# Optimization experiments

Hardware: AMD Instinct MI355X
Metric: run time of the kernel (lower is better)

Reference implementation:

```python
import jax, jax.numpy as jnp
import numpy as np

KNN = 10       # knn_size
TOPK = 4       # top_k_select
H = 4          # num_heads
HID = 64       # edge-MLP hidden dim


def setup_inputs() -> dict:
    key = jax.random.key(0)
    ks = jax.random.split(key, 12)
    B, V, D = 4, 4096, 256
    s = 0.02
    return {
        "voxel_tokens": jax.random.normal(ks[0], (B, V, D), jnp.float32),
        "voxel_coords": jax.random.uniform(ks[1], (B, V, 3), jnp.float32) * 10.0,
        "mask": jnp.ones((B, V), dtype=bool),
        # EdgeScoringMLP: Linear(2D+3 -> 64), Linear(64 -> 1)
        "W1": jax.random.normal(ks[2], (2 * D + 3, HID), jnp.float32) * s,
        "b1": jnp.zeros((HID,), jnp.float32),
        "W2": jax.random.normal(ks[3], (HID, 1), jnp.float32) * s,
        "b2": jnp.zeros((1,), jnp.float32),
        # CrossAttention projections (D -> D)
        "Wq": jax.random.normal(ks[4], (D, D), jnp.float32) * s,
        "bq": jnp.zeros((D,), jnp.float32),
        "Wk": jax.random.normal(ks[5], (D, D), jnp.float32) * s,
        "bk": jnp.zeros((D,), jnp.float32),
        "Wv": jax.random.normal(ks[6], (D, D), jnp.float32) * s,
        "bv": jnp.zeros((D,), jnp.float32),
        "Wo": jax.random.normal(ks[7], (D, D), jnp.float32) * s,
        "bo": jnp.zeros((D,), jnp.float32),
    }


def reference(voxel_tokens, voxel_coords, mask,
              W1, b1, W2, b2, Wq, bq, Wk, bk, Wv, bv, Wo, bo):
    # mask is all-True (Vp == V per batch element), so the original per-batch
    # loop over dynamic voxel counts is an exact vmap over B. Dropouts are in
    # eval mode (identity).
    D = voxel_tokens.shape[-1]
    Dh = D // H

    def single(tok, coo):  # tok: (V, D), coo: (V, 3)
        # --- KNN graph build (squared euclidean; monotonic in true cdist) ---
        sq = jnp.sum(coo * coo, axis=-1)                        # (V,)
        d2 = sq[:, None] + sq[None, :] - 2.0 * (coo @ coo.T)    # (V, V)
        _, knn = jax.lax.top_k(-d2, KNN + 1)                    # smallest dists
        knn = knn[:, 1:]                                        # drop self, (V, KNN)

        # --- edge features: [anchor_tok, neighbor_tok, rel_pos] ---
        nb_tok = tok[knn]                                       # (V, KNN, D)
        rel = coo[knn] - coo[:, None, :]                        # (V, KNN, 3)
        anchor = jnp.broadcast_to(tok[:, None, :], nb_tok.shape)
        ef = jnp.concatenate([anchor, nb_tok, rel], axis=-1)    # (V, KNN, 2D+3)

        # --- edge-MLP scoring + softmax + top-k edge select ---
        sc = (jax.nn.relu(ef @ W1 + b1) @ W2 + b2)[..., 0]      # (V, KNN)
        aw = jax.nn.softmax(sc, axis=-1)
        _, loc = jax.lax.top_k(aw, TOPK)                        # (V, TOPK)
        sel = jnp.take_along_axis(knn, loc, axis=-1)            # (V, TOPK)
        nbr = tok[sel]                                          # (V, TOPK, D)

        # --- cross attention over selected neighbors ---
        Q = (tok @ Wq + bq).reshape(-1, H, Dh)                  # (V, H, Dh)
        K = (nbr @ Wk + bk).reshape(-1, TOPK, H, Dh)            # (V, TOPK, H, Dh)
        Vv = (nbr @ Wv + bv).reshape(-1, TOPK, H, Dh)
        att = jnp.einsum('vhd,vshd->vhs', Q, K) / jnp.sqrt(jnp.float32(Dh))
        w = jax.nn.softmax(att, axis=-1)                        # (V, H, TOPK)
        out = jnp.einsum('vhs,vshd->vhd', w, Vv).reshape(-1, D)
        return out @ Wo + bo                                    # (V, D)

    return jax.vmap(single)(voxel_tokens, voxel_coords)        # (B, V, D)
```

## Files before the change

kernel.cpp:

```cpp
#include <hip/hip_runtime.h>
#include <hip/hip_bf16.h>

#define VV 4096
#define DDIM 256
#define KNN_K 10
#define TK 4

__device__ __forceinline__ float f_sq3(float x, float y, float z) {
    return __fadd_rn(__fadd_rn(__fmul_rn(x, x), __fmul_rn(y, y)), __fmul_rn(z, z));
}
__device__ __forceinline__ float f_dot3(float ax, float ay, float az,
                                        float bx, float by, float bz) {
    float d = __fmul_rn(ax, bx);
    d = __fmaf_rn(ay, by, d);
    d = __fmaf_rn(az, bz, d);
    return d;
}

__device__ __forceinline__ float f_d2(const float* __restrict__ cb, int j, float sqj,
                                      float qx, float qy, float qz, float sqq) {
    float xj = cb[j * 3 + 0], yj = cb[j * 3 + 1], zj = cb[j * 3 + 2];
    float dt = f_dot3(qx, qy, qz, xj, yj, zj);
    return __fsub_rn(__fadd_rn(sqq, sqj), __fmul_rn(2.0f, dt));
}

__device__ __forceinline__ unsigned long long mkkey(float d2, int j) {
    unsigned u = __float_as_uint(d2);
    u ^= (unsigned)((int)u >> 31) | 0x80000000u;
    return ((unsigned long long)u << 32) | (unsigned)j;
}

__global__ void __launch_bounds__(256) an_gemm_kernel(
    const float* __restrict__ tok,
    const float* __restrict__ W1,
    const float* __restrict__ coords,
    float* __restrict__ AN,
    float* __restrict__ sq)
{
    __shared__ float As[16][68];
    __shared__ float Bs[16][68];

    const int mBlock = blockIdx.x * 64;
    const int grp    = blockIdx.y;
    const float* W   = W1 + (size_t)grp * 256 * 64;

    const int tid = threadIdx.x;

    if (grp == 0 && tid < 64) {
        int m = mBlock + tid;
        sq[m] = f_sq3(coords[m * 3 + 0], coords[m * 3 + 1], coords[m * 3 + 2]);
    }

    const int tx = tid & 15;
    const int ty = tid >> 4;

    const int ar  = tid >> 2;
    const int ac4 = tid & 3;
    const int br  = tid >> 4;
    const int bc4 = tid & 15;

    float acc[4][4] = {};

    for (int k0 = 0; k0 < 256; k0 += 16) {
        float4 a4 = *(const float4*)&tok[(size_t)(mBlock + ar) * 256 + k0 + ac4 * 4];
        As[ac4 * 4 + 0][ar] = a4.x;
        As[ac4 * 4 + 1][ar] = a4.y;
        As[ac4 * 4 + 2][ar] = a4.z;
        As[ac4 * 4 + 3][ar] = a4.w;
        float4 b4 = *(const float4*)&W[(size_t)(k0 + br) * 64 + bc4 * 4];
        *(float4*)&Bs[br][bc4 * 4] = b4;
        __syncthreads();
        #pragma unroll
        for (int kk = 0; kk < 16; kk++) {
            float4 av = *(const float4*)&As[kk][ty * 4];
            float4 bv4 = *(const float4*)&Bs[kk][tx * 4];
            acc[0][0] = fmaf(av.x, bv4.x, acc[0][0]); acc[0][1] = fmaf(av.x, bv4.y, acc[0][1]);
            acc[0][2] = fmaf(av.x, bv4.z, acc[0][2]); acc[0][3] = fmaf(av.x, bv4.w, acc[0][3]);
            acc[1][0] = fmaf(av.y, bv4.x, acc[1][0]); acc[1][1] = fmaf(av.y, bv4.y, acc[1][1]);
            acc[1][2] = fmaf(av.y, bv4.z, acc[1][2]); acc[1][3] = fmaf(av.y, bv4.w, acc[1][3]);
            acc[2][0] = fmaf(av.z, bv4.x, acc[2][0]); acc[2][1] = fmaf(av.z, bv4.y, acc[2][1]);
            acc[2][2] = fmaf(av.z, bv4.z, acc[2][2]); acc[2][3] = fmaf(av.z, bv4.w, acc[2][3]);
            acc[3][0] = fmaf(av.w, bv4.x, acc[3][0]); acc[3][1] = fmaf(av.w, bv4.y, acc[3][1]);
            acc[3][2] = fmaf(av.w, bv4.z, acc[3][2]); acc[3][3] = fmaf(av.w, bv4.w, acc[3][3]);
        }
        __syncthreads();
    }

    #pragma unroll
    for (int i = 0; i < 4; i++) {
        int m = mBlock + ty * 4 + i;
        float4 o;
        o.x = acc[i][0]; o.y = acc[i][1]; o.z = acc[i][2]; o.w = acc[i][3];
        *(float4*)&AN[(size_t)m * 128 + grp * 64 + tx * 4] = o;
    }
}

__global__ void __launch_bounds__(256) knn_score_kernel(
    const float* __restrict__ AN,
    const float* __restrict__ coords,
    const float* __restrict__ sq,
    const float* __restrict__ W1,
    const float* __restrict__ b1,
    const float* __restrict__ W2,
    int* __restrict__ sel)
{
    const int tid  = threadIdx.x;
    const int lane = tid & 63;
    const int wave = tid >> 6;
    const int q    = blockIdx.x * 4 + wave;
    const int b    = q >> 12;
    const int v    = q & 4095;
    const int base = q & ~4095;
    const float* cb  = coords + (size_t)b * VV * 3;
    const float* sqb = sq + base;

    __shared__ int   sKnn[4][KNN_K];
    __shared__ float sHid[4][KNN_K][65];
    __shared__ float sSc[4][KNN_K];

    const float qx = cb[v * 3 + 0];
    const float qy = cb[v * 3 + 1];
    const float qz = cb[v * 3 + 2];
    const float sqq = f_sq3(qx, qy, qz);

    unsigned long long best   = ~0ull;
    unsigned long long second = ~0ull;
    unsigned long long used   = 0ull;

    #pragma unroll 4
    for (int i = 0; i < 64; i++) {
        int j = i * 64 + lane;
        unsigned long long k = mkkey(f_d2(cb, j, sqb[j], qx, qy, qz, sqq), j);
        if (k < best) { second = best; best = k; }
        else if (k < second) { second = k; }
    }

    #pragma unroll 1
    for (int it = 0; it < 11; it++) {
        unsigned long long rb = best;
        #pragma unroll
        for (int off = 1; off < 64; off <<= 1) {
            unsigned olo = __shfl_xor((unsigned)rb, off);
            unsigned ohi = __shfl_xor((unsigned)(rb >> 32), off);
            unsigned long long o = ((unsigned long long)ohi << 32) | olo;
            if (o < rb) rb = o;
        }
        int wj = (int)((unsigned)rb & 4095u);
        if (it >= 1 && lane == 0) sKnn[wave][it - 1] = wj;

        if ((unsigned)best == (unsigned)rb) {
            used |= 1ull << (wj >> 6);
            best = second;
            second = ~0ull;
            if (best == ~0ull) {
                #pragma unroll 1
                for (int i = 0; i < 64; i++) {
                    if ((used >> i) & 1ull) continue;
                    int j = i * 64 + lane;
                    unsigned long long k = mkkey(f_d2(cb, j, sqb[j], qx, qy, qz, sqq), j);
                    if (k < best) { second = best; best = k; }
                    else if (k < second) { second = k; }
                }
            }
        }
    }

    const float sAl = AN[(size_t)q * 128 + lane];
    const float b1l = b1[lane];
    const float wr0 = W1[(512 + 0) * 64 + lane];
    const float wr1 = W1[(512 + 1) * 64 + lane];
    const float wr2 = W1[(512 + 2) * 64 + lane];

    #pragma unroll 1
    for (int nb = 0; nb < KNN_K; nb++) {
        int kn = sKnn[wave][nb];
        float acc = __fadd_rn(sAl, AN[(size_t)(base + kn) * 128 + 64 + lane]);
        float rel0 = __fsub_rn(cb[kn * 3 + 0], qx);
        acc = __fmaf_rn(rel0, wr0, acc);
        float rel1 = __fsub_rn(cb[kn * 3 + 1], qy);
        acc = __fmaf_rn(rel1, wr1, acc);
        float rel2 = __fsub_rn(cb[kn * 3 + 2], qz);
        acc = __fmaf_rn(rel2, wr2, acc);
        float hid = __fadd_rn(acc, b1l);
        sHid[wave][nb][lane] = hid > 0.0f ? hid : 0.0f;
    }

    if (lane < KNN_K) {
        float s = 0.0f;
        #pragma unroll 8
        for (int h = 0; h < 64; h++)
            s = __fmaf_rn(sHid[wave][lane][h], W2[h], s);
        sSc[wave][lane] = s;
    }

    if (lane == 0) {
        unsigned um = 0;
        #pragma unroll
        for (int s = 0; s < TK; s++) {
            float bests = -3.4e38f; int bj = 0;
            for (int jj = 0; jj < KNN_K; jj++) {
                if (um & (1u << jj)) continue;
                if (sSc[wave][jj] > bests) { bests = sSc[wave][jj]; bj = jj; }
            }
            um |= 1u << bj;
            sel[(size_t)q * TK + s] = base + sKnn[wave][bj];
        }
    }
}

__global__ void __launch_bounds__(256) qkv_gemm_kernel(
    const float* __restrict__ tok,
    const float* __restrict__ Wq, const float* __restrict__ bq,
    const float* __restrict__ Wk, const float* __restrict__ bk,
    const float* __restrict__ Wv, const float* __restrict__ bv,
    float* __restrict__ qkv)
{
    __shared__ float As[16][68];
    __shared__ float Bs[16][68];

    const int mBlock = blockIdx.x * 64;
    const int nBlock = blockIdx.y * 64;
    const int grp = nBlock >> 8;
    const int nIn = nBlock & 255;
    const float* W    = (grp == 0) ? Wq : (grp == 1) ? Wk : Wv;
    const float* bias = (grp == 0) ? bq : (grp == 1) ? bk : bv;

    const int tid = threadIdx.x;
    const int tx = tid & 15;
    const int ty = tid >> 4;

    const int ar  = tid >> 2;
    const int ac4 = tid & 3;
    const int br  = tid >> 4;
    const int bc4 = tid & 15;

    float acc[4][4] = {};

    for (int k0 = 0; k0 < 256; k0 += 16) {
        float4 a4 = *(const float4*)&tok[(size_t)(mBlock + ar) * 256 + k0 + ac4 * 4];
        As[ac4 * 4 + 0][ar] = a4.x;
        As[ac4 * 4 + 1][ar] = a4.y;
        As[ac4 * 4 + 2][ar] = a4.z;
        As[ac4 * 4 + 3][ar] = a4.w;
        float4 b4 = *(const float4*)&W[(size_t)(k0 + br) * 256 + nIn + bc4 * 4];
        *(float4*)&Bs[br][bc4 * 4] = b4;
        __syncthreads();
        #pragma unroll
        for (int kk = 0; kk < 16; kk++) {
            float4 av = *(const float4*)&As[kk][ty * 4];
            float4 bv4 = *(const float4*)&Bs[kk][tx * 4];
            acc[0][0] = fmaf(av.x, bv4.x, acc[0][0]); acc[0][1] = fmaf(av.x, bv4.y, acc[0][1]);
            acc[0][2] = fmaf(av.x, bv4.z, acc[0][2]); acc[0][3] = fmaf(av.x, bv4.w, acc[0][3]);
            acc[1][0] = fmaf(av.y, bv4.x, acc[1][0]); acc[1][1] = fmaf(av.y, bv4.y, acc[1][1]);
            acc[1][2] = fmaf(av.y, bv4.z, acc[1][2]); acc[1][3] = fmaf(av.y, bv4.w, acc[1][3]);
            acc[2][0] = fmaf(av.z, bv4.x, acc[2][0]); acc[2][1] = fmaf(av.z, bv4.y, acc[2][1]);
            acc[2][2] = fmaf(av.z, bv4.z, acc[2][2]); acc[2][3] = fmaf(av.z, bv4.w, acc[2][3]);
            acc[3][0] = fmaf(av.w, bv4.x, acc[3][0]); acc[3][1] = fmaf(av.w, bv4.y, acc[3][1]);
            acc[3][2] = fmaf(av.w, bv4.z, acc[3][2]); acc[3][3] = fmaf(av.w, bv4.w, acc[3][3]);
        }
        __syncthreads();
    }

    #pragma unroll
    for (int i = 0; i < 4; i++) {
        int m = mBlock + ty * 4 + i;
        float4 o;
        o.x = acc[i][0] + bias[nIn + tx * 4 + 0];
        o.y = acc[i][1] + bias[nIn + tx * 4 + 1];
        o.z = acc[i][2] + bias[nIn + tx * 4 + 2];
        o.w = acc[i][3] + bias[nIn + tx * 4 + 3];
        *(float4*)&qkv[(size_t)m * 768 + nBlock + tx * 4] = o;
    }
}

__global__ void __launch_bounds__(256) attn_gather_kernel(
    const float* __restrict__ qkv, const int* __restrict__ sel,
    float* __restrict__ attnout)
{
    const int q = blockIdx.x;
    const int tid = threadIdx.x;

    const float qv = qkv[(size_t)q * 768 + tid];

    int rows[TK];
    #pragma unroll
    for (int s = 0; s < TK; s++) rows[s] = sel[(size_t)q * TK + s];

    float att[TK];
    #pragma unroll
    for (int s = 0; s < TK; s++) {
        float p = qv * qkv[(size_t)rows[s] * 768 + 256 + tid];
        #pragma unroll
        for (int m = 1; m < 64; m <<= 1) p += __shfl_xor(p, m);
        att[s] = p * 0.125f;
    }

    float mx  = fmaxf(fmaxf(att[0], att[1]), fmaxf(att[2], att[3]));
    float e0 = expf(att[0] - mx), e1 = expf(att[1] - mx),
          e2 = expf(att[2] - mx), e3 = expf(att[3] - mx);
    float inv = 1.0f / (e0 + e1 + e2 + e3);

    float o = (e0 * qkv[(size_t)rows[0] * 768 + 512 + tid] +
               e1 * qkv[(size_t)rows[1] * 768 + 512 + tid] +
               e2 * qkv[(size_t)rows[2] * 768 + 512 + tid] +
               e3 * qkv[(size_t)rows[3] * 768 + 512 + tid]) * inv;

    attnout[(size_t)q * 256 + tid] = o;
}

__global__ void __launch_bounds__(256) wo_gemm_kernel(
    const float* __restrict__ A,
    const float* __restrict__ Wo, const float* __restrict__ bo,
    float* __restrict__ out)
{
    __shared__ float As[16][68];
    __shared__ float Bs[16][68];

    const int mBlock = blockIdx.x * 64;
    const int nBlock = blockIdx.y * 64;

    const int tid = threadIdx.x;
    const int tx = tid & 15;
    const int ty = tid >> 4;

    const int ar  = tid >> 2;
    const int ac4 = tid & 3;
    const int br  = tid >> 4;
    const int bc4 = tid & 15;

    float acc[4][4] = {};

    for (int k0 = 0; k0 < 256; k0 += 16) {
        float4 a4 = *(const float4*)&A[(size_t)(mBlock + ar) * 256 + k0 + ac4 * 4];
        As[ac4 * 4 + 0][ar] = a4.x;
        As[ac4 * 4 + 1][ar] = a4.y;
        As[ac4 * 4 + 2][ar] = a4.z;
        As[ac4 * 4 + 3][ar] = a4.w;
        float4 b4 = *(const float4*)&Wo[(size_t)(k0 + br) * 256 + nBlock + bc4 * 4];
        *(float4*)&Bs[br][bc4 * 4] = b4;
        __syncthreads();
        #pragma unroll
        for (int kk = 0; kk < 16; kk++) {
            float4 av = *(const float4*)&As[kk][ty * 4];
            float4 bv4 = *(const float4*)&Bs[kk][tx * 4];
            acc[0][0] = fmaf(av.x, bv4.x, acc[0][0]); acc[0][1] = fmaf(av.x, bv4.y, acc[0][1]);
            acc[0][2] = fmaf(av.x, bv4.z, acc[0][2]); acc[0][3] = fmaf(av.x, bv4.w, acc[0][3]);
            acc[1][0] = fmaf(av.y, bv4.x, acc[1][0]); acc[1][1] = fmaf(av.y, bv4.y, acc[1][1]);
            acc[1][2] = fmaf(av.y, bv4.z, acc[1][2]); acc[1][3] = fmaf(av.y, bv4.w, acc[1][3]);
            acc[2][0] = fmaf(av.z, bv4.x, acc[2][0]); acc[2][1] = fmaf(av.z, bv4.y, acc[2][1]);
            acc[2][2] = fmaf(av.z, bv4.z, acc[2][2]); acc[2][3] = fmaf(av.z, bv4.w, acc[2][3]);
            acc[3][0] = fmaf(av.w, bv4.x, acc[3][0]); acc[3][1] = fmaf(av.w, bv4.y, acc[3][1]);
            acc[3][2] = fmaf(av.w, bv4.z, acc[3][2]); acc[3][3] = fmaf(av.w, bv4.w, acc[3][3]);
        }
        __syncthreads();
    }

    #pragma unroll
    for (int i = 0; i < 4; i++) {
        int m = mBlock + ty * 4 + i;
        float4 o;
        o.x = acc[i][0] + bo[nBlock + tx * 4 + 0];
        o.y = acc[i][1] + bo[nBlock + tx * 4 + 1];
        o.z = acc[i][2] + bo[nBlock + tx * 4 + 2];
        o.w = acc[i][3] + bo[nBlock + tx * 4 + 3];
        *(float4*)&out[(size_t)m * 256 + nBlock + tx * 4] = o;
    }
}

__global__ void __launch_bounds__(256) fused_voxel_attn(
    const float* __restrict__ tok,
    const float* __restrict__ coords,
    const float* __restrict__ W1,
    const float* __restrict__ b1,
    const float* __restrict__ W2,
    const float* __restrict__ Wq, const float* __restrict__ bq,
    const float* __restrict__ Wk, const float* __restrict__ bk,
    const float* __restrict__ Wv, const float* __restrict__ bv,
    const float* __restrict__ Wo, const float* __restrict__ bo,
    float* __restrict__ out, int out_size)
{
    const int q    = blockIdx.x;
    const int b    = q >> 12;
    const int v    = q & 4095;
    const int base = q & ~4095;
    const int tid  = threadIdx.x;
    const float* cb = coords + (size_t)b * VV * 3;

    __shared__ float  sval[256];
    __shared__ int    sidx[256];
    __shared__ int    sKnn[KNN_K];
    __shared__ int    sSel[TK];
    __shared__ float  sTokA[DDIM];
    __shared__ float  sTokN[KNN_K][DDIM];
    __shared__ float  sAH[64];
    __shared__ float  sHid[KNN_K][64];
    __shared__ float  sSc[KNN_K];
    __shared__ float  sP[TK][256];
    __shared__ float  sAtt[4][TK];
    __shared__ float  sO[DDIM];

    const float qx = cb[v * 3 + 0];
    const float qy = cb[v * 3 + 1];
    const float qz = cb[v * 3 + 2];
    const float sqq = f_sq3(qx, qy, qz);

    float d2[16];
    #pragma unroll
    for (int i = 0; i < 16; i++) {
        int j = tid + i * 256;
        float xj = cb[j * 3 + 0], yj = cb[j * 3 + 1], zj = cb[j * 3 + 2];
        float sqj = f_sq3(xj, yj, zj);
        float dt  = f_dot3(qx, qy, qz, xj, yj, zj);
        d2[i] = __fsub_rn(__fadd_rn(sqq, sqj), __fmul_rn(2.0f, dt));
    }

    unsigned used = 0;
    for (int it = 0; it < 11; it++) {
        float best = 3.4e38f;
// ... 136 lines not shown
                                65536LL, 256LL, 65536LL, 256LL,
                                65536LL, 256LL, 65536LL, 256LL};
    int idx[13];
    const int n = n_in;

    const long long* s64 = (const long long*)(const void*)in_sizes;
    const int*       s32 = in_sizes;

    bool ok = false;

    if (n >= 13 && s64[0] == want[0]) {
        ok = true;
        int walk = 0;
        for (int t = 0; t < 13; t++) {
            int f = -1;
            for (int i = walk; i < n; i++) {
                if (s64[i] == want[t]) { f = i; break; }
            }
            if (f < 0) { ok = false; break; }
            idx[t] = f; walk = f + 1;
        }
    }

    if (!ok) {
        ok = true;
        int walk = 0;
        for (int t = 0; t < 13; t++) {
            int f = -1;
            for (int i = walk; i < n; i++) {
                if ((long long)s32[i] == want[t]) { f = i; break; }
            }
            if (f < 0) { ok = false; break; }
            idx[t] = f; walk = f + 1;
        }
    }

    if (!ok) return;

    const float* tok    = (const float*)d_in[idx[0]];
    const float* coords = (const float*)d_in[idx[1]];
    const float* W1     = (const float*)d_in[idx[2]];
    const float* b1     = (const float*)d_in[idx[3]];
    const float* W2     = (const float*)d_in[idx[4]];
    const float* Wq     = (const float*)d_in[idx[5]];
    const float* bq     = (const float*)d_in[idx[6]];
    const float* Wk     = (const float*)d_in[idx[7]];
    const float* bk     = (const float*)d_in[idx[8]];
    const float* Wv     = (const float*)d_in[idx[9]];
    const float* bv     = (const float*)d_in[idx[10]];
    const float* Wo     = (const float*)d_in[idx[11]];
    const float* bo     = (const float*)d_in[idx[12]];
    float* out = (float*)d_out;

    const size_t NEED = 67436544;
    if (ws_size >= NEED) {
        char* ws = (char*)d_ws;
        int*   sel     = (int*)  (ws + 0);
        float* AN      = (float*)(ws + 262144);
        float* attnout = (float*)(ws + 262144);
        float* qkv     = (float*)(ws + 17039360);
        float* sq      = (float*)(ws + 67371008);

        an_gemm_kernel<<<dim3(256, 2), dim3(256), 0, stream>>>(tok, W1, coords, AN, sq);
        knn_score_kernel<<<dim3(4096), dim3(256), 0, stream>>>(AN, coords, sq, W1, b1, W2, sel);
        qkv_gemm_kernel<<<dim3(256, 12), dim3(256), 0, stream>>>(tok, Wq, bq, Wk, bk, Wv, bv, qkv);
        attn_gather_kernel<<<dim3(16384), dim3(256), 0, stream>>>(qkv, sel, attnout);
        wo_gemm_kernel<<<dim3(256, 4), dim3(256), 0, stream>>>(attnout, Wo, bo, out);
    } else {
        fused_voxel_attn<<<dim3(16384), dim3(256), 0, stream>>>(
            tok, coords, W1, b1, W2, Wq, bq, Wk, bk, Wv, bv, Wo, bo, out, out_size);
    }
}
```

Before: 373.0 us.

## Merge KNN scoring and QKV GEMM into one launch, pack coords as float4

Packs each voxel's coordinates and squared norm into a single float4 so the brute-force KNN scan does one vector load per candidate instead of four scalar loads. The KNN/scoring blocks and the QKV projection GEMM become one heterogeneous kernel, interleaving 16 KNN blocks with 3 GEMM blocks per group so the compute-heavy GEMM can overlap the latency-bound KNN scan. The QKV and Wo GEMMs switch from 64x64 to 128x128 tiles with 2x2 register sub-tiles for more reuse per shared-memory load. The cost is higher register pressure in the merged kernel, which may lower occupancy for the KNN path, and fewer blocks for the Wo GEMM.

```diff
diff --git a/kernel.cpp b/kernel.cpp
--- a/kernel.cpp
+++ b/kernel.cpp
@@ -17,13 +17,6 @@
     return d;
 }
 
-__device__ __forceinline__ float f_d2(const float* __restrict__ cb, int j, float sqj,
-                                      float qx, float qy, float qz, float sqq) {
-    float xj = cb[j * 3 + 0], yj = cb[j * 3 + 1], zj = cb[j * 3 + 2];
-    float dt = f_dot3(qx, qy, qz, xj, yj, zj);
-    return __fsub_rn(__fadd_rn(sqq, sqj), __fmul_rn(2.0f, dt));
-}
-
 __device__ __forceinline__ unsigned long long mkkey(float d2, int j) {
     unsigned u = __float_as_uint(d2);
     u ^= (unsigned)((int)u >> 31) | 0x80000000u;
@@ -35,7 +28,7 @@
     const float* __restrict__ W1,
     const float* __restrict__ coords,
     float* __restrict__ AN,
-    float* __restrict__ sq)
+    float4* __restrict__ cxyzs)
 {
     __shared__ float As[16][68];
     __shared__ float Bs[16][68];
@@ -48,7 +41,8 @@
 
     if (grp == 0 && tid < 64) {
         int m = mBlock + tid;
-        sq[m] = f_sq3(coords[m * 3 + 0], coords[m * 3 + 1], coords[m * 3 + 2]);
+        float x = coords[m * 3 + 0], y = coords[m * 3 + 1], z = coords[m * 3 + 2];
+        cxyzs[m] = make_float4(x, y, z, f_sq3(x, y, z));
     }
 
     const int tx = tid & 15;
@@ -95,181 +89,204 @@
     }
 }
 
-__global__ void __launch_bounds__(256) knn_score_kernel(
+__global__ void __launch_bounds__(256) knn_qkv_kernel(
     const float* __restrict__ AN,
-    const float* __restrict__ coords,
-    const float* __restrict__ sq,
+    const float4* __restrict__ cxyzs,
     const float* __restrict__ W1,
     const float* __restrict__ b1,
     const float* __restrict__ W2,
-    int* __restrict__ sel)
-{
-    const int tid  = threadIdx.x;
-    const int lane = tid & 63;
-    const int wave = tid >> 6;
-    const int q    = blockIdx.x * 4 + wave;
-    const int b    = q >> 12;
-    const int v    = q & 4095;
-    const int base = q & ~4095;
-    const float* cb  = coords + (size_t)b * VV * 3;
-    const float* sqb = sq + base;
-
-    __shared__ int   sKnn[4][KNN_K];
-    __shared__ float sHid[4][KNN_K][65];
-    __shared__ float sSc[4][KNN_K];
-
-    const float qx = cb[v * 3 + 0];
-    const float qy = cb[v * 3 + 1];
-    const float qz = cb[v * 3 + 2];
-    const float sqq = f_sq3(qx, qy, qz);
-
-    unsigned long long best   = ~0ull;
-    unsigned long long second = ~0ull;
-    unsigned long long used   = 0ull;
-
-    #pragma unroll 4
-    for (int i = 0; i < 64; i++) {
-        int j = i * 64 + lane;
-        unsigned long long k = mkkey(f_d2(cb, j, sqb[j], qx, qy, qz, sqq), j);
-        if (k < best) { second = best; best = k; }
-        else if (k < second) { second = k; }
-    }
-
-    #pragma unroll 1
-    for (int it = 0; it < 11; it++) {
-        unsigned long long rb = best;
-        #pragma unroll
-        for (int off = 1; off < 64; off <<= 1) {
-            unsigned olo = __shfl_xor((unsigned)rb, off);
-            unsigned ohi = __shfl_xor((unsigned)(rb >> 32), off);
-            unsigned long long o = ((unsigned long long)ohi << 32) | olo;
-            if (o < rb) rb = o;
-        }
-        int wj = (int)((unsigned)rb & 4095u);
-        if (it >= 1 && lane == 0) sKnn[wave][it - 1] = wj;
-
-        if ((unsigned)best == (unsigned)rb) {
-            used |= 1ull << (wj >> 6);
-            best = second;
-            second = ~0ull;
-            if (best == ~0ull) {
-                #pragma unroll 1
-                for (int i = 0; i < 64; i++) {
-                    if ((used >> i) & 1ull) continue;
-                    int j = i * 64 + lane;
-                    unsigned long long k = mkkey(f_d2(cb, j, sqb[j], qx, qy, qz, sqq), j);
-                    if (k < best) { second = best; best = k; }
-                    else if (k < second) { second = k; }
-                }
-            }
-        }
-    }
-
-    const float sAl = AN[(size_t)q * 128 + lane];
-    const float b1l = b1[lane];
-    const float wr0 = W1[(512 + 0) * 64 + lane];
-    const float wr1 = W1[(512 + 1) * 64 + lane];
-    const float wr2 = W1[(512 + 2) * 64 + lane];
-
-    #pragma unroll 1
-    for (int nb = 0; nb < KNN_K; nb++) {
-        int kn = sKnn[wave][nb];
-        float acc = __fadd_rn(sAl, AN[(size_t)(base + kn) * 128 + 64 + lane]);
-        float rel0 = __fsub_rn(cb[kn * 3 + 0], qx);
-        acc = __fmaf_rn(rel0, wr0, acc);
-        float rel1 = __fsub_rn(cb[kn * 3 + 1], qy);
-        acc = __fmaf_rn(rel1, wr1, acc);
-        float rel2 = __fsub_rn(cb[kn * 3 + 2], qz);
-        acc = __fmaf_rn(rel2, wr2, acc);
-        float hid = __fadd_rn(acc, b1l);
-        sHid[wave][nb][lane] = hid > 0.0f ? hid : 0.0f;
-    }
-
-    if (lane < KNN_K) {
-        float s = 0.0f;
-        #pragma unroll 8
-        for (int h = 0; h < 64; h++)
-            s = __fmaf_rn(sHid[wave][lane][h], W2[h], s);
-        sSc[wave][lane] = s;
-    }
-
-    if (lane == 0) {
-        unsigned um = 0;
-        #pragma unroll
-        for (int s = 0; s < TK; s++) {
-            float bests = -3.4e38f; int bj = 0;
-            for (int jj = 0; jj < KNN_K; jj++) {
-                if (um & (1u << jj)) continue;
-                if (sSc[wave][jj] > bests) { bests = sSc[wave][jj]; bj = jj; }
-            }
-            um |= 1u << bj;
-            sel[(size_t)q * TK + s] = base + sKnn[wave][bj];
-        }
-    }
-}
-
-__global__ void __launch_bounds__(256) qkv_gemm_kernel(
+    int* __restrict__ sel,
     const float* __restrict__ tok,
     const float* __restrict__ Wq, const float* __restrict__ bq,
     const float* __restrict__ Wk, const float* __restrict__ bk,
     const float* __restrict__ Wv, const float* __restrict__ bv,
     float* __restrict__ qkv)
 {
-    __shared__ float As[16][68];
-    __shared__ float Bs[16][68];
-
-    const int mBlock = blockIdx.x * 64;
-    const int nBlock = blockIdx.y * 64;
-    const int grp = nBlock >> 8;
-    const int nIn = nBlock & 255;
-    const float* W    = (grp == 0) ? Wq : (grp == 1) ? Wk : Wv;
-    const float* bias = (grp == 0) ? bq : (grp == 1) ? bk : bv;
-
-    const int tid = threadIdx.x;
-    const int tx = tid & 15;
-    const int ty = tid >> 4;
-
-    const int ar  = tid >> 2;
-    const int ac4 = tid & 3;
-    const int br  = tid >> 4;
-    const int bc4 = tid & 15;
-
-    float acc[4][4] = {};
-
-    for (int k0 = 0; k0 < 256; k0 += 16) {
-        float4 a4 = *(const float4*)&tok[(size_t)(mBlock + ar) * 256 + k0 + ac4 * 4];
-        As[ac4 * 4 + 0][ar] = a4.x;
-        As[ac4 * 4 + 1][ar] = a4.y;
-        As[ac4 * 4 + 2][ar] = a4.z;
-        As[ac4 * 4 + 3][ar] = a4.w;
-        float4 b4 = *(const float4*)&W[(size_t)(k0 + br) * 256 + nIn + bc4 * 4];
-        *(float4*)&Bs[br][bc4 * 4] = b4;
-        __syncthreads();
-        #pragma unroll
-        for (int kk = 0; kk < 16; kk++) {
-            float4 av = *(const float4*)&As[kk][ty * 4];
-            float4 bv4 = *(const float4*)&Bs[kk][tx * 4];
-            acc[0][0] = fmaf(av.x, bv4.x, acc[0][0]); acc[0][1] = fmaf(av.x, bv4.y, acc[0][1]);
-            acc[0][2] = fmaf(av.x, bv4.z, acc[0][2]); acc[0][3] = fmaf(av.x, bv4.w, acc[0][3]);
-            acc[1][0] = fmaf(av.y, bv4.x, acc[1][0]); acc[1][1] = fmaf(av.y, bv4.y, acc[1][1]);
-            acc[1][2] = fmaf(av.y, bv4.z, acc[1][2]); acc[1][3] = fmaf(av.y, bv4.w, acc[1][3]);
-            acc[2][0] = fmaf(av.z, bv4.x, acc[2][0]); acc[2][1] = fmaf(av.z, bv4.y, acc[2][1]);
-            acc[2][2] = fmaf(av.z, bv4.z, acc[2][2]); acc[2][3] = fmaf(av.z, bv4.w, acc[2][3]);
-            acc[3][0] = fmaf(av.w, bv4.x, acc[3][0]); acc[3][1] = fmaf(av.w, bv4.y, acc[3][1]);
-            acc[3][2] = fmaf(av.w, bv4.z, acc[3][2]); acc[3][3] = fmaf(av.w, bv4.w, acc[3][3]);
-        }
-        __syncthreads();
-    }
-
-    #pragma unroll
-    for (int i = 0; i < 4; i++) {
-        int m = mBlock + ty * 4 + i;
-        float4 o;
-        o.x = acc[i][0] + bias[nIn + tx * 4 + 0];
-        o.y = acc[i][1] + bias[nIn + tx * 4 + 1];
-        o.z = acc[i][2] + bias[nIn + tx * 4 + 2];
-        o.w = acc[i][3] + bias[nIn + tx * 4 + 3];
-        *(float4*)&qkv[(size_t)m * 768 + nBlock + tx * 4] = o;
+    __shared__ __align__(16) char smem[16896];
+    const int tid   = threadIdx.x;
+    const int g     = blockIdx.x;
+    const int group = g / 19;
+    const int rem   = g - group * 19;
+
+    if (rem < 16) {
+        const int kb   = group * 16 + rem;
+        const int lane = tid & 63;
+        const int wave = tid >> 6;
+        const int q    = kb * 4 + wave;
+        const int base = q & ~4095;
+        const int v    = q & 4095;
+        const float4* cx = cxyzs + base;
+
+        int*   sKnn = (int*)smem;
+        float* sSc  = (float*)(smem + 160);
+        float* sHid = (float*)(smem + 320);
+
+        float4 cq = cx[v];
+        const float qx = cq.x, qy = cq.y, qz = cq.z, sqq = cq.w;
+
+        unsigned long long best   = ~0ull;
+        unsigned long long second = ~0ull;
+        unsigned long long used   = 0ull;
+
+        #pragma unroll 4
+        for (int i = 0; i < 64; i++) {
+            int j = i * 64 + lane;
+            float4 c = cx[j];
+            float dt  = f_dot3(qx, qy, qz, c.x, c.y, c.z);
+            float d2v = __fsub_rn(__fadd_rn(sqq, c.w), __fmul_rn(2.0f, dt));
+            unsigned long long k = mkkey(d2v, j);
+            if (k < best) { second = best; best = k; }
+            else if (k < second) { second = k; }
+        }
+
+        #pragma unroll 1
+        for (int it = 0; it < 11; it++) {
+            unsigned long long rb = best;
+            #pragma unroll
+            for (int off = 1; off < 64; off <<= 1) {
+                unsigned olo = __shfl_xor((unsigned)rb, off);
+                unsigned ohi = __shfl_xor((unsigned)(rb >> 32), off);
+                unsigned long long o = ((unsigned long long)ohi << 32) | olo;
+                if (o < rb) rb = o;
+            }
+            int wj = (int)((unsigned)rb & 4095u);
+            if (it >= 1 && lane == 0) sKnn[wave * KNN_K + it - 1] = wj;
+
+            if ((unsigned)best == (unsigned)rb) {
+                used |= 1ull << (wj >> 6);
+                best = second;
+                second = ~0ull;
+                if (best == ~0ull) {
+                    #pragma unroll 1
+                    for (int i = 0; i < 64; i++) {
+                        if ((used >> i) & 1ull) continue;
+                        int j = i * 64 + lane;
+                        float4 c = cx[j];
+                        float dt  = f_dot3(qx, qy, qz, c.x, c.y, c.z);
+                        float d2v = __fsub_rn(__fadd_rn(sqq, c.w), __fmul_rn(2.0f, dt));
+                        unsigned long long k = mkkey(d2v, j);
+                        if (k < best) { second = best; best = k; }
+                        else if (k < second) { second = k; }
+                    }
+                }
+            }
+        }
+
+        const float sAl = AN[(size_t)q * 128 + lane];
+        const float b1l = b1[lane];
+        const float wr0 = W1[(512 + 0) * 64 + lane];
+        const float wr1 = W1[(512 + 1) * 64 + lane];
+        const float wr2 = W1[(512 + 2) * 64 + lane];
+
+        #pragma unroll 1
+        for (int nb = 0; nb < KNN_K; nb++) {
+            int kn = sKnn[wave * KNN_K + nb];
+            float4 cn = cx[kn];
+            float acc = __fadd_rn(sAl, AN[(size_t)(base + kn) * 128 + 64 + lane]);
+            float rel0 = __fsub_rn(cn.x, qx);
+            acc = __fmaf_rn(rel0, wr0, acc);
+            float rel1 = __fsub_rn(cn.y, qy);
+            acc = __fmaf_rn(rel1, wr1, acc);
+            float rel2 = __fsub_rn(cn.z, qz);
+            acc = __fmaf_rn(rel2, wr2, acc);
+            float hid = __fadd_rn(acc, b1l);
+            sHid[(wave * KNN_K + nb) * 65 + lane] = hid > 0.0f ? hid : 0.0f;
+        }
+
+        if (lane < KNN_K) {
+            float s = 0.0f;
+            #pragma unroll 8
+            for (int h = 0; h < 64; h++)
+                s = __fmaf_rn(sHid[(wave * KNN_K + lane) * 65 + h], W2[h], s);
+            sSc[wave * KNN_K + lane] = s;
+        }
+
+        if (lane == 0) {
+            unsigned um = 0;
+            #pragma unroll
+            for (int s = 0; s < TK; s++) {
+                float bests = -3.4e38f; int bj = 0;
+                for (int jj = 0; jj < KNN_K; jj++) {
+                    if (um & (1u << jj)) continue;
+                    float sc = sSc[wave * KNN_K + jj];
+                    if (sc > bests) { bests = sc; bj = jj; }
+                }
+                um |= 1u << bj;
+                sel[(size_t)q * TK + s] = base + sKnn[wave * KNN_K + bj];
+            }
+        }
+    } else {
+        float* As = (float*)smem;
+        float* Bs = (float*)smem + 16 * 132;
+
+        const int id     = group * 3 + (rem - 16);
+        const int mBlock = (id & 127) * 128;
+        const int nb     = id >> 7;
+        const int grp    = nb >> 1;
+        const int nIn    = (nb & 1) * 128;
+        const float* W    = (grp == 0) ? Wq : (grp == 1) ? Wk : Wv;
+        const float* bias = (grp == 0) ? bq : (grp == 1) ? bk : bv;
+
+        const int tx = tid & 15;
+        const int ty = tid >> 4;
+        const int ar  = tid >> 2;
+        const int ac4 = tid & 3;
+        const int br  = tid >> 4;
+        const int bc4 = tid & 15;
+
+        float acc[2][2][4][4] = {};
+
+        for (int k0 = 0; k0 < 256; k0 += 16) {
+            float4 a0 = *(const float4*)&tok[(size_t)(mBlock + ar) * 256 + k0 + ac4 * 4];
+            float4 a1 = *(const float4*)&tok[(size_t)(mBlock + 64 + ar) * 256 + k0 + ac4 * 4];
+            As[(ac4 * 4 + 0) * 132 + ar] = a0.x;      As[(ac4 * 4 + 0) * 132 + 64 + ar] = a1.x;
+            As[(ac4 * 4 + 1) * 132 + ar] = a0.y;      As[(ac4 * 4 + 1) * 132 + 64 + ar] = a1.y;
+            As[(ac4 * 4 + 2) * 132 + ar] = a0.z;      As[(ac4 * 4 + 2) * 132 + 64 + ar] = a1.z;
+            As[(ac4 * 4 + 3) * 132 + ar] = a0.w;      As[(ac4 * 4 + 3) * 132 + 64 + ar] = a1.w;
+            float4 b0 = *(const float4*)&W[(size_t)(k0 + br) * 256 + nIn + bc4 * 4];
+            float4 b1v = *(const float4*)&W[(size_t)(k0 + br) * 256 + nIn + 64 + bc4 * 4];
+            *(float4*)&Bs[br * 132 + bc4 * 4] = b0;
+            *(float4*)&Bs[br * 132 + 64 + bc4 * 4] = b1v;
+            __syncthreads();
+            #pragma unroll
+            for (int kk = 0; kk < 16; kk++) {
+                float4 av0 = *(const float4*)&As[kk * 132 + ty * 4];
+                float4 av1 = *(const float4*)&As[kk * 132 + 64 + ty * 4];
+                float4 bv0 = *(const float4*)&Bs[kk * 132 + tx * 4];
+                float4 bv1 = *(const float4*)&Bs[kk * 132 + 64 + tx * 4];
+                const float am[2][4] = {{av0.x, av0.y, av0.z, av0.w},
+                                        {av1.x, av1.y, av1.z, av1.w}};
+                const float bn[2][4] = {{bv0.x, bv0.y, bv0.z, bv0.w},
+                                        {bv1.x, bv1.y, bv1.z, bv1.w}};
+                #pragma unroll
+                for (int mi = 0; mi < 2; mi++)
+                #pragma unroll
+                for (int i = 0; i < 4; i++)
+                #pragma unroll
+                for (int ni = 0; ni < 2; ni++)
+                #pragma unroll
+                for (int j = 0; j < 4; j++)
+                    acc[mi][ni][i][j] = fmaf(am[mi][i], bn[ni][j], acc[mi][ni][i][j]);
+            }
+            __syncthreads();
+        }
+
+        #pragma unroll
+        for (int mi = 0; mi < 2; mi++)
+        #pragma unroll
+        for (int i = 0; i < 4; i++) {
+            int m = mBlock + mi * 64 + ty * 4 + i;
+            #pragma unroll
+            for (int ni = 0; ni < 2; ni++) {
+                int col = nIn + ni * 64 + tx * 4;
+                float4 o;
+                o.x = acc[mi][ni][i][0] + bias[col + 0];
+                o.y = acc[mi][ni][i][1] + bias[col + 1];
+                o.z = acc[mi][ni][i][2] + bias[col + 2];
+                o.w = acc[mi][ni][i][3] + bias[col + 3];
+                *(float4*)&qkv[(size_t)m * 768 + grp * 256 + col] = o;
+            }
+        }
     }
 }
 
@@ -313,57 +330,72 @@
     const float* __restrict__ Wo, const float* __restrict__ bo,
     float* __restrict__ out)
 {
-    __shared__ float As[16][68];
-    __shared__ float Bs[16][68];
-
-    const int mBlock = blockIdx.x * 64;
-    const int nBlock = blockIdx.y * 64;
+    __shared__ float As[16][132];
+    __shared__ float Bs[16][132];
+
+    const int mBlock = blockIdx.x * 128;
+    const int nBlock = blockIdx.y * 128;
 
     const int tid = threadIdx.x;
     const int tx = tid & 15;
     const int ty = tid >> 4;
-
     const int ar  = tid >> 2;
     const int ac4 = tid & 3;
     const int br  = tid >> 4;
     const int bc4 = tid & 15;
 
-    float acc[4][4] = {};
+    float acc[2][2][4][4] = {};
 
     for (int k0 = 0; k0 < 256; k0 += 16) {
-        float4 a4 = *(const float4*)&A[(size_t)(mBlock + ar) * 256 + k0 + ac4 * 4];
-        As[ac4 * 4 + 0][ar] = a4.x;
-        As[ac4 * 4 + 1][ar] = a4.y;
-        As[ac4 * 4 + 2][ar] = a4.z;
-        As[ac4 * 4 + 3][ar] = a4.w;
-        float4 b4 = *(const float4*)&Wo[(size_t)(k0 + br) * 256 + nBlock + bc4 * 4];
-        *(float4*)&Bs[br][bc4 * 4] = b4;
+        float4 a0 = *(const float4*)&A[(size_t)(mBlock + ar) * 256 + k0 + ac4 * 4];
+        float4 a1 = *(const float4*)&A[(size_t)(mBlock + 64 + ar) * 256 + k0 + ac4 * 4];
+        As[ac4 * 4 + 0][ar] = a0.x;      As[ac4 * 4 + 0][64 + ar] = a1.x;
+        As[ac4 * 4 + 1][ar] = a0.y;      As[ac4 * 4 + 1][64 + ar] = a1.y;
+        As[ac4 * 4 + 2][ar] = a0.z;      As[ac4 * 4 + 2][64 + ar] = a1.z;
+        As[ac4 * 4 + 3][ar] = a0.w;      As[ac4 * 4 + 3][64 + ar] = a1.w;
+        float4 b0 = *(const float4*)&Wo[(size_t)(k0 + br) * 256 + nBlock + bc4 * 4];
+        float4 b1v = *(const float4*)&Wo[(size_t)(k0 + br) * 256 + nBlock + 64 + bc4 * 4];
+        *(float4*)&Bs[br][bc4 * 4] = b0;
+        *(float4*)&Bs[br][64 + bc4 * 4] = b1v;
         __syncthreads();
         #pragma unroll
         for (int kk = 0; kk < 16; kk++) {
-            float4 av = *(const float4*)&As[kk][ty * 4];
-            float4 bv4 = *(const float4*)&Bs[kk][tx * 4];
-            acc[0][0] = fmaf(av.x, bv4.x, acc[0][0]); acc[0][1] = fmaf(av.x, bv4.y, acc[0][1]);
-            acc[0][2] = fmaf(av.x, bv4.z, acc[0][2]); acc[0][3] = fmaf(av.x, bv4.w, acc[0][3]);
-            acc[1][0] = fmaf(av.y, bv4.x, acc[1][0]); acc[1][1] = fmaf(av.y, bv4.y, acc[1][1]);
-            acc[1][2] = fmaf(av.y, bv4.z, acc[1][2]); acc[1][3] = fmaf(av.y, bv4.w, acc[1][3]);
-            acc[2][0] = fmaf(av.z, bv4.x, acc[2][0]); acc[2][1] = fmaf(av.z, bv4.y, acc[2][1]);
-            acc[2][2] = fmaf(av.z, bv4.z, acc[2][2]); acc[2][3] = fmaf(av.z, bv4.w, acc[2][3]);
-            acc[3][0] = fmaf(av.w, bv4.x, acc[3][0]); acc[3][1] = fmaf(av.w, bv4.y, acc[3][1]);
-            acc[3][2] = fmaf(av.w, bv4.z, acc[3][2]); acc[3][3] = fmaf(av.w, bv4.w, acc[3][3]);
+            float4 av0 = *(const float4*)&As[kk][ty * 4];
+            float4 av1 = *(const float4*)&As[kk][64 + ty * 4];
+            float4 bv0 = *(const float4*)&Bs[kk][tx * 4];
+            float4 bv1 = *(const float4*)&Bs[kk][64 + tx * 4];
+            const float am[2][4] = {{av0.x, av0.y, av0.z, av0.w},
+                                    {av1.x, av1.y, av1.z, av1.w}};
+            const float bn[2][4] = {{bv0.x, bv0.y, bv0.z, bv0.w},
+                                    {bv1.x, bv1.y, bv1.z, bv1.w}};
+            #pragma unroll
+            for (int mi = 0; mi < 2; mi++)
+            #pragma unroll
+            for (int i = 0; i < 4; i++)
+            #pragma unroll
+            for (int ni = 0; ni < 2; ni++)
+            #pragma unroll
+            for (int j = 0; j < 4; j++)
+                acc[mi][ni][i][j] = fmaf(am[mi][i], bn[ni][j], acc[mi][ni][i][j]);
         }
         __syncthreads();
     }
 
     #pragma unroll
+    for (int mi = 0; mi < 2; mi++)
+    #pragma unroll
     for (int i = 0; i < 4; i++) {
-        int m = mBlock + ty * 4 + i;
-        float4 o;
-        o.x = acc[i][0] + bo[nBlock + tx * 4 + 0];
-        o.y = acc[i][1] + bo[nBlock + tx * 4 + 1];
-        o.z = acc[i][2] + bo[nBlock + tx * 4 + 2];
-        o.w = acc[i][3] + bo[nBlock + tx * 4 + 3];
-        *(float4*)&out[(size_t)m * 256 + nBlock + tx * 4] = o;
+        int m = mBlock + mi * 64 + ty * 4 + i;
+        #pragma unroll
+        for (int ni = 0; ni < 2; ni++) {
+            int col = nBlock + ni * 64 + tx * 4;
+            float4 o;
+            o.x = acc[mi][ni][i][0] + bo[col + 0];
+            o.y = acc[mi][ni][i][1] + bo[col + 1];
+            o.z = acc[mi][ni][i][2] + bo[col + 2];
+            o.w = acc[mi][ni][i][3] + bo[col + 3];
+            *(float4*)&out[(size_t)m * 256 + col] = o;
+        }
     }
 }
 
@@ -606,20 +638,20 @@
     const float* bo     = (const float*)d_in[idx[12]];
     float* out = (float*)d_out;
 
-    const size_t NEED = 67436544;
+    const size_t NEED = 67633152;
     if (ws_size >= NEED) {
         char* ws = (char*)d_ws;
-        int*   sel     = (int*)  (ws + 0);
-        float* AN      = (float*)(ws + 262144);
-        float* attnout = (float*)(ws + 262144);
-        float* qkv     = (float*)(ws + 17039360);
-        float* sq      = (float*)(ws + 67371008);
-
-        an_gemm_kernel<<<dim3(256, 2), dim3(256), 0, stream>>>(tok, W1, coords, AN, sq);
-        knn_score_kernel<<<dim3(4096), dim3(256), 0, stream>>>(AN, coords, sq, W1, b1, W2, sel);
-        qkv_gemm_kernel<<<dim3(256, 12), dim3(256), 0, stream>>>(tok, Wq, bq, Wk, bk, Wv, bv, qkv);
+        int*    sel     = (int*)   (ws + 0);
+        float*  AN      = (float*) (ws + 262144);
+        float*  attnout = (float*) (ws + 262144);
+        float*  qkv     = (float*) (ws + 17039360);
+        float4* cxyzs   = (float4*)(ws + 67371008);
+
+        an_gemm_kernel<<<dim3(256, 2), dim3(256), 0, stream>>>(tok, W1, coords, AN, cxyzs);
+        knn_qkv_kernel<<<dim3(4864), dim3(256), 0, stream>>>(
+            AN, cxyzs, W1, b1, W2, sel, tok, Wq, bq, Wk, bk, Wv, bv, qkv);
         attn_gather_kernel<<<dim3(16384), dim3(256), 0, stream>>>(qkv, sel, attnout);
-        wo_gemm_kernel<<<dim3(256, 4), dim3(256), 0, stream>>>(attnout, Wo, bo, out);
+        wo_gemm_kernel<<<dim3(128, 2), dim3(256), 0, stream>>>(attnout, Wo, bo, out);
     } else {
         fused_voxel_attn<<<dim3(16384), dim3(256), 0, stream>>>(
             tok, coords, W1, b1, W2, Wq, bq, Wk, bk, Wv, bv, Wo, bo, out, out_size);
```

After: 374.4 us. No clear change (+0.4%).

## Merge QKV and edge-MLP GEMMs into one launch; pack coords with squared norm

Applied to the files above, without the earlier changes.

The QKV projection GEMM and the anchor/neighbor edge-MLP GEMM now run in a single launch with 14 column-block groups, so there is one fewer kernel launch and a larger grid to fill the GPU. Coordinates are precomputed as float4 (x, y, z, |c|^2), so the KNN scan does one vectorized load per candidate instead of four scalar loads. This costs extra workspace and some branching inside the GEMM kernel.

```diff
diff --git a/kernel.cpp b/kernel.cpp
--- a/kernel.cpp
+++ b/kernel.cpp
@@ -17,39 +17,55 @@
     return d;
 }
 
-__device__ __forceinline__ float f_d2(const float* __restrict__ cb, int j, float sqj,
-                                      float qx, float qy, float qz, float sqq) {
-    float xj = cb[j * 3 + 0], yj = cb[j * 3 + 1], zj = cb[j * 3 + 2];
-    float dt = f_dot3(qx, qy, qz, xj, yj, zj);
-    return __fsub_rn(__fadd_rn(sqq, sqj), __fmul_rn(2.0f, dt));
-}
-
 __device__ __forceinline__ unsigned long long mkkey(float d2, int j) {
     unsigned u = __float_as_uint(d2);
     u ^= (unsigned)((int)u >> 31) | 0x80000000u;
     return ((unsigned long long)u << 32) | (unsigned)j;
 }
 
-__global__ void __launch_bounds__(256) an_gemm_kernel(
+__device__ __forceinline__ void fma44(const float4 a, const float4 b, float (&c)[4][4]) {
+    c[0][0] = fmaf(a.x, b.x, c[0][0]); c[0][1] = fmaf(a.x, b.y, c[0][1]);
+    c[0][2] = fmaf(a.x, b.z, c[0][2]); c[0][3] = fmaf(a.x, b.w, c[0][3]);
+    c[1][0] = fmaf(a.y, b.x, c[1][0]); c[1][1] = fmaf(a.y, b.y, c[1][1]);
+    c[1][2] = fmaf(a.y, b.z, c[1][2]); c[1][3] = fmaf(a.y, b.w, c[1][3]);
+    c[2][0] = fmaf(a.z, b.x, c[2][0]); c[2][1] = fmaf(a.z, b.y, c[2][1]);
+    c[2][2] = fmaf(a.z, b.z, c[2][2]); c[2][3] = fmaf(a.z, b.w, c[2][3]);
+    c[3][0] = fmaf(a.w, b.x, c[3][0]); c[3][1] = fmaf(a.w, b.y, c[3][1]);
+    c[3][2] = fmaf(a.w, b.z, c[3][2]); c[3][3] = fmaf(a.w, b.w, c[3][3]);
+}
+
+__global__ void __launch_bounds__(256) qkv_an_gemm_kernel(
     const float* __restrict__ tok,
+    const float* __restrict__ Wq, const float* __restrict__ bq,
+    const float* __restrict__ Wk, const float* __restrict__ bk,
+    const float* __restrict__ Wv, const float* __restrict__ bv,
     const float* __restrict__ W1,
     const float* __restrict__ coords,
+    float* __restrict__ qkv,
     float* __restrict__ AN,
-    float* __restrict__ sq)
+    float4* __restrict__ cxyzs)
 {
     __shared__ float As[16][68];
     __shared__ float Bs[16][68];
 
     const int mBlock = blockIdx.x * 64;
-    const int grp    = blockIdx.y;
-    const float* W   = W1 + (size_t)grp * 256 * 64;
-
-    const int tid = threadIdx.x;
-
-    if (grp == 0 && tid < 64) {
+    const int by     = blockIdx.y;
+    const int tid    = threadIdx.x;
+    const bool isAN  = (by >= 12);
+    const int  half  = by - 12;
+
+    if (by == 13 && tid < 64) {
         int m = mBlock + tid;
-        sq[m] = f_sq3(coords[m * 3 + 0], coords[m * 3 + 1], coords[m * 3 + 2]);
-    }
+        float x = coords[m * 3 + 0], y = coords[m * 3 + 1], z = coords[m * 3 + 2];
+        cxyzs[m] = make_float4(x, y, z, f_sq3(x, y, z));
+    }
+
+    const int nBlock = isAN ? 0 : by * 64;
+    const int grp    = isAN ? 0 : (nBlock >> 8);
+    const int nIn    = nBlock & 255;
+    const float* W    = isAN ? (W1 + (size_t)half * 256 * 64)
+                             : ((grp == 0) ? Wq : (grp == 1) ? Wk : Wv);
+    const float* bias = (grp == 0) ? bq : (grp == 1) ? bk : bv;
 
     const int tx = tid & 15;
     const int ty = tid >> 4;
@@ -67,38 +83,45 @@
         As[ac4 * 4 + 1][ar] = a4.y;
         As[ac4 * 4 + 2][ar] = a4.z;
         As[ac4 * 4 + 3][ar] = a4.w;
-        float4 b4 = *(const float4*)&W[(size_t)(k0 + br) * 64 + bc4 * 4];
+        float4 b4;
+        if (isAN) b4 = *(const float4*)&W[(size_t)(k0 + br) * 64 + bc4 * 4];
+        else      b4 = *(const float4*)&W[(size_t)(k0 + br) * 256 + nIn + bc4 * 4];
         *(float4*)&Bs[br][bc4 * 4] = b4;
         __syncthreads();
         #pragma unroll
         for (int kk = 0; kk < 16; kk++) {
             float4 av = *(const float4*)&As[kk][ty * 4];
             float4 bv4 = *(const float4*)&Bs[kk][tx * 4];
-            acc[0][0] = fmaf(av.x, bv4.x, acc[0][0]); acc[0][1] = fmaf(av.x, bv4.y, acc[0][1]);
-            acc[0][2] = fmaf(av.x, bv4.z, acc[0][2]); acc[0][3] = fmaf(av.x, bv4.w, acc[0][3]);
-            acc[1][0] = fmaf(av.y, bv4.x, acc[1][0]); acc[1][1] = fmaf(av.y, bv4.y, acc[1][1]);
-            acc[1][2] = fmaf(av.y, bv4.z, acc[1][2]); acc[1][3] = fmaf(av.y, bv4.w, acc[1][3]);
-            acc[2][0] = fmaf(av.z, bv4.x, acc[2][0]); acc[2][1] = fmaf(av.z, bv4.y, acc[2][1]);
-            acc[2][2] = fmaf(av.z, bv4.z, acc[2][2]); acc[2][3] = fmaf(av.z, bv4.w, acc[2][3]);
-            acc[3][0] = fmaf(av.w, bv4.x, acc[3][0]); acc[3][1] = fmaf(av.w, bv4.y, acc[3][1]);
-            acc[3][2] = fmaf(av.w, bv4.z, acc[3][2]); acc[3][3] = fmaf(av.w, bv4.w, acc[3][3]);
+            fma44(av, bv4, acc);
         }
         __syncthreads();
     }
 
-    #pragma unroll
-    for (int i = 0; i < 4; i++) {
-        int m = mBlock + ty * 4 + i;
-        float4 o;
-        o.x = acc[i][0]; o.y = acc[i][1]; o.z = acc[i][2]; o.w = acc[i][3];
-        *(float4*)&AN[(size_t)m * 128 + grp * 64 + tx * 4] = o;
+    if (!isAN) {
+        #pragma unroll
+        for (int i = 0; i < 4; i++) {
+            int m = mBlock + ty * 4 + i;
+            float4 o;
+            o.x = acc[i][0] + bias[nIn + tx * 4 + 0];
+            o.y = acc[i][1] + bias[nIn + tx * 4 + 1];
+            o.z = acc[i][2] + bias[nIn + tx * 4 + 2];
+            o.w = acc[i][3] + bias[nIn + tx * 4 + 3];
+            *(float4*)&qkv[(size_t)m * 768 + nBlock + tx * 4] = o;
+        }
+    } else {
+        #pragma unroll
+        for (int i = 0; i < 4; i++) {
+            int m = mBlock + ty * 4 + i;
+            float4 o;
+            o.x = acc[i][0]; o.y = acc[i][1]; o.z = acc[i][2]; o.w = acc[i][3];
+            *(float4*)&AN[(size_t)m * 128 + half * 64 + tx * 4] = o;
+        }
     }
 }
 
 __global__ void __launch_bounds__(256) knn_score_kernel(
     const float* __restrict__ AN,
-    const float* __restrict__ coords,
-    const float* __restrict__ sq,
+    const float4* __restrict__ cxyzs,
     const float* __restrict__ W1,
     const float* __restrict__ b1,
     const float* __restrict__ W2,
@@ -108,20 +131,16 @@
     const int lane = tid & 63;
     const int wave = tid >> 6;
     const int q    = blockIdx.x * 4 + wave;
-    const int b    = q >> 12;
+    const int base = q & ~4095;
     const int v    = q & 4095;
-    const int base = q & ~4095;
-    const float* cb  = coords + (size_t)b * VV * 3;
-    const float* sqb = sq + base;
+    const float4* cx = cxyzs + base;
 
     __shared__ int   sKnn[4][KNN_K];
+    __shared__ float sSc[4][KNN_K];
     __shared__ float sHid[4][KNN_K][65];
-    __shared__ float sSc[4][KNN_K];
-
-    const float qx = cb[v * 3 + 0];
-    const float qy = cb[v * 3 + 1];
-    const float qz = cb[v * 3 + 2];
-    const float sqq = f_sq3(qx, qy, qz);
+
+    float4 cq = cx[v];
+    const float qx = cq.x, qy = cq.y, qz = cq.z, sqq = cq.w;
 
     unsigned long long best   = ~0ull;
     unsigned long long second = ~0ull;
@@ -130,7 +149,10 @@
     #pragma unroll 4
     for (int i = 0; i < 64; i++) {
         int j = i * 64 + lane;
-        unsigned long long k = mkkey(f_d2(cb, j, sqb[j], qx, qy, qz, sqq), j);
+        float4 c = cx[j];
+        float dt  = f_dot3(qx, qy, qz, c.x, c.y, c.z);
+        float d2v = __fsub_rn(__fadd_rn(sqq, c.w), __fmul_rn(2.0f, dt));
+        unsigned long long k = mkkey(d2v, j);
         if (k < best) { second = best; best = k; }
         else if (k < second) { second = k; }
     }
@@ -157,7 +179,10 @@
                 for (int i = 0; i < 64; i++) {
                     if ((used >> i) & 1ull) continue;
                     int j = i * 64 + lane;
-                    unsigned long long k = mkkey(f_d2(cb, j, sqb[j], qx, qy, qz, sqq), j);
+                    float4 c = cx[j];
+                    float dt  = f_dot3(qx, qy, qz, c.x, c.y, c.z);
+                    float d2v = __fsub_rn(__fadd_rn(sqq, c.w), __fmul_rn(2.0f, dt));
+                    unsigned long long k = mkkey(d2v, j);
                     if (k < best) { second = best; best = k; }
                     else if (k < second) { second = k; }
                 }
@@ -174,12 +199,13 @@
     #pragma unroll 1
     for (int nb = 0; nb < KNN_K; nb++) {
         int kn = sKnn[wave][nb];
+        float4 cn = cx[kn];
         float acc = __fadd_rn(sAl, AN[(size_t)(base + kn) * 128 + 64 + lane]);
-        float rel0 = __fsub_rn(cb[kn * 3 + 0], qx);
+        float rel0 = __fsub_rn(cn.x, qx);
         acc = __fmaf_rn(rel0, wr0, acc);
-        float rel1 = __fsub_rn(cb[kn * 3 + 1], qy);
+        float rel1 = __fsub_rn(cn.y, qy);
         acc = __fmaf_rn(rel1, wr1, acc);
-        float rel2 = __fsub_rn(cb[kn * 3 + 2], qz);
+        float rel2 = __fsub_rn(cn.z, qz);
         acc = __fmaf_rn(rel2, wr2, acc);
         float hid = __fadd_rn(acc, b1l);
         sHid[wave][nb][lane] = hid > 0.0f ? hid : 0.0f;
@@ -200,76 +226,12 @@
             float bests = -3.4e38f; int bj = 0;
             for (int jj = 0; jj < KNN_K; jj++) {
                 if (um & (1u << jj)) continue;
-                if (sSc[wave][jj] > bests) { bests = sSc[wave][jj]; bj = jj; }
+                float sc = sSc[wave][jj];
+                if (sc > bests) { bests = sc; bj = jj; }
             }
             um |= 1u << bj;
             sel[(size_t)q * TK + s] = base + sKnn[wave][bj];
         }
-    }
-}
-
-__global__ void __launch_bounds__(256) qkv_gemm_kernel(
-    const float* __restrict__ tok,
-    const float* __restrict__ Wq, const float* __restrict__ bq,
-    const float* __restrict__ Wk, const float* __restrict__ bk,
-    const float* __restrict__ Wv, const float* __restrict__ bv,
-    float* __restrict__ qkv)
-{
-    __shared__ float As[16][68];
-    __shared__ float Bs[16][68];
-
-    const int mBlock = blockIdx.x * 64;
-    const int nBlock = blockIdx.y * 64;
-    const int grp = nBlock >> 8;
-    const int nIn = nBlock & 255;
-    const float* W    = (grp == 0) ? Wq : (grp == 1) ? Wk : Wv;
-    const float* bias = (grp == 0) ? bq : (grp == 1) ? bk : bv;
-
-    const int tid = threadIdx.x;
-    const int tx = tid & 15;
-    const int ty = tid >> 4;
-
-    const int ar  = tid >> 2;
-    const int ac4 = tid & 3;
-    const int br  = tid >> 4;
-    const int bc4 = tid & 15;
-
-    float acc[4][4] = {};
-
-    for (int k0 = 0; k0 < 256; k0 += 16) {
-        float4 a4 = *(const float4*)&tok[(size_t)(mBlock + ar) * 256 + k0 + ac4 * 4];
-        As[ac4 * 4 + 0][ar] = a4.x;
-        As[ac4 * 4 + 1][ar] = a4.y;
-        As[ac4 * 4 + 2][ar] = a4.z;
-        As[ac4 * 4 + 3][ar] = a4.w;
-        float4 b4 = *(const float4*)&W[(size_t)(k0 + br) * 256 + nIn + bc4 * 4];
-        *(float4*)&Bs[br][bc4 * 4] = b4;
-        __syncthreads();
-        #pragma unroll
-        for (int kk = 0; kk < 16; kk++) {
-            float4 av = *(const float4*)&As[kk][ty * 4];
-            float4 bv4 = *(const float4*)&Bs[kk][tx * 4];
-            acc[0][0] = fmaf(av.x, bv4.x, acc[0][0]); acc[0][1] = fmaf(av.x, bv4.y, acc[0][1]);
-            acc[0][2] = fmaf(av.x, bv4.z, acc[0][2]); acc[0][3] = fmaf(av.x, bv4.w, acc[0][3]);
-            acc[1][0] = fmaf(av.y, bv4.x, acc[1][0]); acc[1][1] = fmaf(av.y, bv4.y, acc[1][1]);
-            acc[1][2] = fmaf(av.y, bv4.z, acc[1][2]); acc[1][3] = fmaf(av.y, bv4.w, acc[1][3]);
-            acc[2][0] = fmaf(av.z, bv4.x, acc[2][0]); acc[2][1] = fmaf(av.z, bv4.y, acc[2][1]);
-            acc[2][2] = fmaf(av.z, bv4.z, acc[2][2]); acc[2][3] = fmaf(av.z, bv4.w, acc[2][3]);
-            acc[3][0] = fmaf(av.w, bv4.x, acc[3][0]); acc[3][1] = fmaf(av.w, bv4.y, acc[3][1]);
-            acc[3][2] = fmaf(av.w, bv4.z, acc[3][2]); acc[3][3] = fmaf(av.w, bv4.w, acc[3][3]);
-        }
-        __syncthreads();
-    }
-
-    #pragma unroll
-    for (int i = 0; i < 4; i++) {
-        int m = mBlock + ty * 4 + i;
-        float4 o;
-        o.x = acc[i][0] + bias[nIn + tx * 4 + 0];
-        o.y = acc[i][1] + bias[nIn + tx * 4 + 1];
-        o.z = acc[i][2] + bias[nIn + tx * 4 + 2];
-        o.w = acc[i][3] + bias[nIn + tx * 4 + 3];
-        *(float4*)&qkv[(size_t)m * 768 + nBlock + tx * 4] = o;
     }
 }
 
@@ -343,14 +305,7 @@
         for (int kk = 0; kk < 16; kk++) {
             float4 av = *(const float4*)&As[kk][ty * 4];
             float4 bv4 = *(const float4*)&Bs[kk][tx * 4];
-            acc[0][0] = fmaf(av.x, bv4.x, acc[0][0]); acc[0][1] = fmaf(av.x, bv4.y, acc[0][1]);
-            acc[0][2] = fmaf(av.x, bv4.z, acc[0][2]); acc[0][3] = fmaf(av.x, bv4.w, acc[0][3]);
-            acc[1][0] = fmaf(av.y, bv4.x, acc[1][0]); acc[1][1] = fmaf(av.y, bv4.y, acc[1][1]);
-            acc[1][2] = fmaf(av.y, bv4.z, acc[1][2]); acc[1][3] = fmaf(av.y, bv4.w, acc[1][3]);
-            acc[2][0] = fmaf(av.z, bv4.x, acc[2][0]); acc[2][1] = fmaf(av.z, bv4.y, acc[2][1]);
-            acc[2][2] = fmaf(av.z, bv4.z, acc[2][2]); acc[2][3] = fmaf(av.z, bv4.w, acc[2][3]);
-            acc[3][0] = fmaf(av.w, bv4.x, acc[3][0]); acc[3][1] = fmaf(av.w, bv4.y, acc[3][1]);
-            acc[3][2] = fmaf(av.w, bv4.z, acc[3][2]); acc[3][3] = fmaf(av.w, bv4.w, acc[3][3]);
+            fma44(av, bv4, acc);
         }
         __syncthreads();
     }
@@ -606,18 +561,18 @@
     const float* bo     = (const float*)d_in[idx[12]];
     float* out = (float*)d_out;
 
-    const size_t NEED = 67436544;
+    const size_t NEED = 67633152;
     if (ws_size >= NEED) {
         char* ws = (char*)d_ws;
-        int*   sel     = (int*)  (ws + 0);
-        float* AN      = (float*)(ws + 262144);
-        float* attnout = (float*)(ws + 262144);
-        float* qkv     = (float*)(ws + 17039360);
-        float* sq      = (float*)(ws + 67371008);
-
-        an_gemm_kernel<<<dim3(256, 2), dim3(256), 0, stream>>>(tok, W1, coords, AN, sq);
-        knn_score_kernel<<<dim3(4096), dim3(256), 0, stream>>>(AN, coords, sq, W1, b1, W2, sel);
-        qkv_gemm_kernel<<<dim3(256, 12), dim3(256), 0, stream>>>(tok, Wq, bq, Wk, bk, Wv, bv, qkv);
+        int*    sel     = (int*)   (ws + 0);
+        float*  AN      = (float*) (ws + 262144);
+        float*  attnout = (float*) (ws + 262144);
+        float*  qkv     = (float*) (ws + 17039360);
+        float4* cxyzs   = (float4*)(ws + 67371008);
+
+        qkv_an_gemm_kernel<<<dim3(256, 14), dim3(256), 0, stream>>>(
+            tok, Wq, bq, Wk, bk, Wv, bv, W1, coords, qkv, AN, cxyzs);
+        knn_score_kernel<<<dim3(4096), dim3(256), 0, stream>>>(AN, cxyzs, W1, b1, W2, sel);
         attn_gather_kernel<<<dim3(16384), dim3(256), 0, stream>>>(qkv, sel, attnout);
         wo_gemm_kernel<<<dim3(256, 4), dim3(256), 0, stream>>>(attnout, Wo, bo, out);
     } else {
```

Result: no change. 367.8 us (-1.4%).
